# Optimization experiments

Measured on AMD Instinct MI355X. Metric: run time of the kernel, lower is better.

Reference implementation:

```python
import jax, jax.numpy as jnp
import numpy as np

K_PERIODS = 4
PMAX = 64
MIN_PERIOD = 8


def setup_inputs() -> dict:
    key = jax.random.key(0)
    x = jax.random.normal(key, (32, 512, 64), dtype=jnp.float32)  # [B, T, N]
    return {"x": x}


def reference(x):
    """Dense, fixed-shape equivalent of PeriodicityTransform.forward (mask=None).

    Instead of a Python list of variable-shape PeriodGroup tiles, returns a
    padded tensor values[bn, k, c, p] where for each (sequence bn, freq rank k)
    with period P and cycles C, values[bn, k, :C, :P] equals the torch tile
    seqs[bn, T-C*P : T].reshape(C, P); entries outside (C, P) are zero.
    Also returns the integer periods and cycles per (bn, k).
    """
    B, T, N = x.shape
    BN = B * N
    seqs = jnp.transpose(x, (0, 2, 1)).reshape(BN, T)  # [BN, T]

    # top-k nonzero FFT frequencies (DC bin zeroed out)
    spec = jnp.fft.rfft(seqs, axis=-1)
    mag2 = spec.real ** 2 + spec.imag ** 2
    mag2 = mag2.at[..., 0].set(0.0)
    _, kidx = jax.lax.top_k(mag2, K_PERIODS)  # [BN, K]
    kidx = jnp.maximum(kidx, 1)

    # periods = clamp(T // f, min=MIN_PERIOD, max=PMAX); cycles = T // period
    periods = jnp.clip(T // kidx, MIN_PERIOD, PMAX)  # [BN, K]
    cycles = T // periods                              # [BN, K]

    cmax = T // MIN_PERIOD  # static upper bound on cycles
    i = jnp.arange(cmax)[:, None]   # cycle index  [Cmax, 1]
    j = jnp.arange(PMAX)[None, :]   # phase index  [1, Pmax]

    start = T - cycles * periods                                   # [BN, K]
    idx = start[..., None, None] + i * periods[..., None, None] + j  # [BN,K,Cmax,Pmax]
    idx = jnp.clip(idx, 0, T - 1)
    valid = (i < cycles[..., None, None]) & (j < periods[..., None, None])

    gathered = jnp.take_along_axis(
        seqs[:, None, :], idx.reshape(BN, K_PERIODS, -1), axis=-1
    ).reshape(BN, K_PERIODS, cmax, PMAX)
    values = jnp.where(valid, gathered, jnp.float32(0.0))
    return values, periods, cycles
```

## Files before the change

### kernel.cpp

```cpp
#include <hip/hip_runtime.h>
#include <math.h>

#define TT 512
#define KP 4

typedef unsigned long long u64;

#define SYNCL() asm volatile("s_waitcnt lgkmcnt(0)\n\ts_barrier" ::: "memory")
#define SYNCW() do { asm volatile("s_waitcnt lgkmcnt(0)" ::: "memory"); \
                     __builtin_amdgcn_sched_barrier(0); } while (0)

__global__ __launch_bounds__(256) void periodicity_kernel(const float* __restrict__ x,
                                                          float* __restrict__ out) {
    const int bn   = (blockIdx.x & 7) * 256 + (blockIdx.x >> 3);
    const int tid  = threadIdx.x;
    const int lane = tid & 63;
    const int wid  = tid >> 6;
    const int b = bn >> 6;
    const int n = bn & 63;

    __shared__ float2 tw[TT];
    __shared__ __align__(16) float row[TT];
    __shared__ __align__(16) float2 buf[TT];
    __shared__ __align__(16) u64 keys[256];
    __shared__ double candV8[8];

    float sv, cv;
    sincosf((float)(2.0 * M_PI / 512.0) * (float)tid, &sv, &cv);
    tw[tid]       = make_float2(cv, -sv);
    tw[tid + 256] = make_float2(-cv, sv);

    const float* xb = x + (size_t)b * (TT * 64) + n;
    {
        float v0 = xb[(size_t)tid * 64];
        float v1 = xb[(size_t)(tid + 256) * 64];
        row[tid] = v0;  row[tid + 256] = v1;
        float sum = v0 + v1, dif = v0 - v1;
        buf[tid]       = make_float2(sum, 0.f);
        buf[tid + 256] = make_float2(dif * cv, -dif * sv);
    }
    SYNCL();

    if (wid < 2) {
        const int h = wid;
        float2* bb = &buf[h << 8];

        #pragma unroll
        for (int stg = 0; stg < 3; ++stg) {
            const int Q  = 64 >> (2 * stg);
            const int g  = lane >> (6 - 2 * stg);
            const int i  = lane & (Q - 1);
            const int base = g * (Q << 2) + i;
            float2 x0 = bb[base],         x1 = bb[base + Q];
            float2 x2 = bb[base + 2 * Q], x3 = bb[base + 3 * Q];
            float2 A  = make_float2(x0.x + x2.x, x0.y + x2.y);
            float2 Bm = make_float2(x0.x - x2.x, x0.y - x2.y);
            float2 Cc = make_float2(x1.x + x3.x, x1.y + x3.y);
            float2 D  = make_float2(x1.x - x3.x, x1.y - x3.y);
            float2 y0 = make_float2(A.x + Cc.x, A.y + Cc.y);
            float2 y2 = make_float2(A.x - Cc.x, A.y - Cc.y);
            float2 y1 = make_float2(Bm.x + D.y, Bm.y - D.x);
            float2 y3 = make_float2(Bm.x - D.y, Bm.y + D.x);
            const int m = i << (1 + 2 * stg);
            float2 t1 = tw[m], t2 = tw[2 * m], t3 = tw[3 * m];
            bb[base]         = y0;
            bb[base + Q]     = make_float2(y1.x * t1.x - y1.y * t1.y, y1.x * t1.y + y1.y * t1.x);
            bb[base + 2 * Q] = make_float2(y2.x * t2.x - y2.y * t2.y, y2.x * t2.y + y2.y * t2.x);
            bb[base + 3 * Q] = make_float2(y3.x * t3.x - y3.y * t3.y, y3.x * t3.y + y3.y * t3.x);
            SYNCW();
        }

        {
            const int g = lane;
            const int base = g << 2;
            float2 x0 = bb[base],     x1 = bb[base + 1];
            float2 x2 = bb[base + 2], x3 = bb[base + 3];
            float2 A  = make_float2(x0.x + x2.x, x0.y + x2.y);
            float2 Bm = make_float2(x0.x - x2.x, x0.y - x2.y);
            float2 Cc = make_float2(x1.x + x3.x, x1.y + x3.y);
            float2 D  = make_float2(x1.x - x3.x, x1.y - x3.y);
            float2 y0 = make_float2(A.x + Cc.x, A.y + Cc.y);
            float2 y2 = make_float2(A.x - Cc.x, A.y - Cc.y);
            float2 y1 = make_float2(Bm.x + D.y, Bm.y - D.x);
            float2 y3 = make_float2(Bm.x - D.y, Bm.y + D.x);
            const int revg = ((g & 3) << 4) | (((g >> 2) & 3) << 2) | ((g >> 4) & 3);
            const int f0 = 2 * revg + h;
            float m0 = y0.x * y0.x + y0.y * y0.y;
            float m1 = y1.x * y1.x + y1.y * y1.y;
            float m2 = y2.x * y2.x + y2.y * y2.y;
            float m3 = y3.x * y3.x + y3.y * y3.y;
            u64 kA, kB;
            if (f0 == 0) {
                kA = ((u64)__float_as_uint(m1) << 32) | (u64)(256 - 128);
                kB = ((u64)__float_as_uint(m2) << 32) | (u64)(256 - 256);
            } else {
                kA = ((u64)__float_as_uint(m0) << 32) | (u64)(256 - f0);
                kB = ((u64)__float_as_uint(m1) << 32) | (u64)(256 - (f0 + 128));
            }
            ulonglong2* kv = (ulonglong2*)keys;
            kv[(h << 6) + g] = make_ulonglong2(kA, kB);
        }
    }
    SYNCL();

    int   fbin[8];
    float cmag[8];
    {
        const ulonglong2* kv = (const ulonglong2*)keys;
        ulonglong2 p0v = kv[lane * 2];
        ulonglong2 p1v = kv[lane * 2 + 1];
        u64 k0 = p0v.x, k1 = p0v.y, k2 = p1v.x, k3 = p1v.y;
        #define CSWAP(a, b) { if (a < b) { u64 _t = a; a = b; b = _t; } }
        CSWAP(k0, k1) CSWAP(k2, k3) CSWAP(k0, k2) CSWAP(k1, k3) CSWAP(k1, k2)
        #undef CSWAP
        #pragma unroll
        for (int r = 0; r < 8; ++r) {
            u64 w = k0;
            #pragma unroll
            for (int off = 32; off >= 1; off >>= 1) {
                u64 o = __shfl_xor(w, off);
                if (o > w) w = o;
            }
            if (k0 == w) { k0 = k1; k1 = k2; k2 = k3; k3 = 0; }
            fbin[r] = 256 - (int)(w & 0xff);
            cmag[r] = __uint_as_float((unsigned)(w >> 32));
        }
    }

    int per[KP], cycv[KP], stv[KP];
    {
        const bool needRefine =
            ((cmag[0] - cmag[1]) <= 1e-4f * cmag[0]) || ((cmag[1] - cmag[2]) <= 1e-4f * cmag[1]) ||
            ((cmag[2] - cmag[3]) <= 1e-4f * cmag[2]) || ((cmag[3] - cmag[4]) <= 1e-4f * cmag[3]);
        int bins[KP];
        if (!needRefine) {
            #pragma unroll
            for (int k = 0; k < KP; ++k) bins[k] = fbin[k];
        } else {
            {
                const int cid = tid >> 5;
                const int sub = tid & 31;
                int fc;
                switch (cid) {
                    case 0: fc = fbin[0]; break;
                    case 1: fc = fbin[1]; break;
                    case 2: fc = fbin[2]; break;
                    case 3: fc = fbin[3]; break;
                    case 4: fc = fbin[4]; break;
                    case 5: fc = fbin[5]; break;
                    case 6: fc = fbin[6]; break;
                    default: fc = fbin[7]; break;
                }
                const int t0 = sub * 16;
                const double W = 6.2831853071795864769 / 512.0;
                double zr, zi, wr, wi;
                sincos(W * (double)((fc * t0) & 511), &zi, &zr);
                sincos(W * (double)fc, &wi, &wr);
                double ar = 0.0, ai = 0.0;
                const float4* r4 = (const float4*)row;
                #pragma unroll
                for (int v4i = 0; v4i < 4; ++v4i) {
                    float4 xv = r4[sub * 4 + v4i];
                    #define STEP(comp)                                   \
                        { double xd = (double)xv.comp;                   \
                          ar = fma(xd, zr, ar); ai = fma(xd, zi, ai);    \
                          double tq = zr * wr - zi * wi;                 \
                          zi = fma(zr, wi, zi * wr); zr = tq; }
                    STEP(x) STEP(y) STEP(z) STEP(w)
                    #undef STEP
                }
                #pragma unroll
                for (int off = 16; off >= 1; off >>= 1) {
                    ar += __shfl_xor(ar, off);
                    ai += __shfl_xor(ai, off);
                }
                if (sub == 0) candV8[cid] = ar * ar + ai * ai;
            }
            SYNCL();
            unsigned chosen = 0;
            #pragma unroll
            for (int k = 0; k < KP; ++k) {
                double bv = -1.0; int bbin = 0x7fffffff; int bj = 0;
                #pragma unroll
                for (int j = 0; j < 8; ++j) {
                    if (chosen & (1u << j)) continue;
                    double vj = candV8[j];
                    int    bjn = fbin[j];
                    if (vj > bv || (vj == bv && bjn < bbin)) { bv = vj; bbin = bjn; bj = j; }
                }
                chosen |= (1u << bj);
                bins[k] = bbin;
            }
        }
        #pragma unroll
        for (int k = 0; k < KP; ++k) {
            int p = TT / bins[k];
            p = p < 8 ? 8 : (p > 64 ? 64 : p);
            per[k]  = p;
            cycv[k] = TT / p;
            stv[k]  = TT - cycv[k] * p;
        }
    }

    const size_t VOFF = (size_t)2048 * KP * 64 * 64;
    if (tid == 0) {
        #pragma unroll
        for (int k = 0; k < KP; ++k) {
            out[VOFF + (size_t)bn * KP + k]        = (float)per[k];
            out[VOFF + 8192 + (size_t)bn * KP + k] = (float)cycv[k];
        }
    }

    float* outv = out + (size_t)bn * (KP * 64 * 64);
    const int c_local = tid >> 4;
    const int p0 = (tid & 15) << 2;
    #pragma unroll
    for (int it = 0; it < 16; ++it) {
        const int k = it >> 2;
        const int c = ((it & 3) << 4) + c_local;
        float4 v = make_float4(0.f, 0.f, 0.f, 0.f);
        const int P = per[k], C = cycv[k], S0 = stv[k];
        if (c < C) {
            const int base = S0 + c * P;
            if (p0 + 3 < P) {
                v.x = row[base + p0];
                v.y = row[base + p0 + 1];
                v.z = row[base + p0 + 2];
                v.w = row[base + p0 + 3];
            } else {
                if (p0     < P) v.x = row[base + p0];
                if (p0 + 1 < P) v.y = row[base + p0 + 1];
                if (p0 + 2 < P) v.z = row[base + p0 + 2];
                if (p0 + 3 < P) v.w = row[base + p0 + 3];
            }
        }
        *(float4*)(outv + (size_t)it * 1024 + (size_t)tid * 4) = v;
    }
}

extern "C" void kernel_launch(void* const* d_in, const int* in_sizes, int n_in,
                              void* d_out, int out_size, void* d_ws, size_t ws_size,
                              hipStream_t stream) {
    const float* x = (const float*)d_in[0];
    float* out = (float*)d_out;
    hipLaunchKernelGGL(periodicity_kernel, dim3(2048), dim3(256), 0, stream, x, out);
}
```

Baseline: 30.48 us.

## Process four sequences per block with warp-specialized FFT/output software pipeline

Each block now handles four consecutive sequences with 512 threads. Two waves prefetch the next sequence and run the FFT and top-k, while six waves write the output tiles for the previous sequence from double-buffered shared memory. The refinement path is moved into a single wave using shuffles instead of a block barrier. This aims to overlap output stores with FFT compute and amortize twiddle setup, at the cost of fewer blocks (512) and extra barriers per stage.

```diff
diff --git a/kernel.cpp b/kernel.cpp
--- a/kernel.cpp
+++ b/kernel.cpp
@@ -10,136 +10,195 @@
 #define SYNCW() do { asm volatile("s_waitcnt lgkmcnt(0)" ::: "memory"); \
                      __builtin_amdgcn_sched_barrier(0); } while (0)
 
-__global__ __launch_bounds__(256) void periodicity_kernel(const float* __restrict__ x,
-                                                          float* __restrict__ out) {
-    const int bn   = (blockIdx.x & 7) * 256 + (blockIdx.x >> 3);
+__global__ __launch_bounds__(512, 4) void periodicity_kernel(const float* __restrict__ x,
+                                                             float* __restrict__ out) {
+    const int bid  = blockIdx.x;
+    const int blk  = (bid & 7) * 64 + (bid >> 3);
     const int tid  = threadIdx.x;
     const int lane = tid & 63;
     const int wid  = tid >> 6;
-    const int b = bn >> 6;
-    const int n = bn & 63;
 
     __shared__ float2 tw[TT];
-    __shared__ __align__(16) float row[TT];
+    __shared__ __align__(16) float rowl[2][TT];
     __shared__ __align__(16) float2 buf[TT];
     __shared__ __align__(16) u64 keys[256];
-    __shared__ double candV8[8];
-
-    float sv, cv;
-    sincosf((float)(2.0 * M_PI / 512.0) * (float)tid, &sv, &cv);
-    tw[tid]       = make_float2(cv, -sv);
-    tw[tid + 256] = make_float2(-cv, sv);
-
-    const float* xb = x + (size_t)b * (TT * 64) + n;
+    __shared__ int pst[2][12];
+
+    const int b  = blk >> 4;
+    const int n0 = (blk & 15) << 2;
+    const size_t VOFF = (size_t)2048 * KP * 64 * 64;
+
+    float cur[8], nxt[8];
+    const float* xb = x + (size_t)b * (TT * 64);
+    if (wid < 2) {
+        const float* xc = xb + n0;
+        #pragma unroll
+        for (int q = 0; q < 8; ++q) cur[q] = xc[(size_t)(lane + 64 * q) * 64];
+    }
+
     {
-        float v0 = xb[(size_t)tid * 64];
-        float v1 = xb[(size_t)(tid + 256) * 64];
-        row[tid] = v0;  row[tid + 256] = v1;
-        float sum = v0 + v1, dif = v0 - v1;
-        buf[tid]       = make_float2(sum, 0.f);
-        buf[tid + 256] = make_float2(dif * cv, -dif * sv);
+        float s, c;
+        sincosf((float)(2.0 * M_PI / 512.0) * (float)tid, &s, &c);
+        tw[tid] = make_float2(c, -s);
     }
     SYNCL();
 
-    if (wid < 2) {
-        const int h = wid;
-        float2* bb = &buf[h << 8];
-
-        #pragma unroll
-        for (int stg = 0; stg < 3; ++stg) {
-            const int Q  = 64 >> (2 * stg);
-            const int g  = lane >> (6 - 2 * stg);
-            const int i  = lane & (Q - 1);
-            const int base = g * (Q << 2) + i;
-            float2 x0 = bb[base],         x1 = bb[base + Q];
-            float2 x2 = bb[base + 2 * Q], x3 = bb[base + 3 * Q];
-            float2 A  = make_float2(x0.x + x2.x, x0.y + x2.y);
-            float2 Bm = make_float2(x0.x - x2.x, x0.y - x2.y);
-            float2 Cc = make_float2(x1.x + x3.x, x1.y + x3.y);
-            float2 D  = make_float2(x1.x - x3.x, x1.y - x3.y);
-            float2 y0 = make_float2(A.x + Cc.x, A.y + Cc.y);
-            float2 y2 = make_float2(A.x - Cc.x, A.y - Cc.y);
-            float2 y1 = make_float2(Bm.x + D.y, Bm.y - D.x);
-            float2 y3 = make_float2(Bm.x - D.y, Bm.y + D.x);
-            const int m = i << (1 + 2 * stg);
-            float2 t1 = tw[m], t2 = tw[2 * m], t3 = tw[3 * m];
-            bb[base]         = y0;
-            bb[base + Q]     = make_float2(y1.x * t1.x - y1.y * t1.y, y1.x * t1.y + y1.y * t1.x);
-            bb[base + 2 * Q] = make_float2(y2.x * t2.x - y2.y * t2.y, y2.x * t2.y + y2.y * t2.x);
-            bb[base + 3 * Q] = make_float2(y3.x * t3.x - y3.y * t3.y, y3.x * t3.y + y3.y * t3.x);
+    for (int r = 0; r < 5; ++r) {
+        const int slot = r & 1, pslot = slot ^ 1;
+
+        if (wid < 2 && r < 4) {
+            const int h = wid;
+            if (r < 3) {
+                const float* xc = xb + (n0 + r + 1);
+                #pragma unroll
+                for (int q = 0; q < 8; ++q) nxt[q] = xc[(size_t)(lane + 64 * q) * 64];
+            }
+            if (h == 0) {
+                #pragma unroll
+                for (int q = 0; q < 4; ++q) rowl[slot][lane + 64 * q] = cur[q];
+            } else {
+                #pragma unroll
+                for (int q = 0; q < 4; ++q) rowl[slot][256 + lane + 64 * q] = cur[4 + q];
+            }
+            if (h == 0) {
+                #pragma unroll
+                for (int q = 0; q < 4; ++q)
+                    buf[lane + 64 * q] = make_float2(cur[q] + cur[4 + q], 0.f);
+            } else {
+                #pragma unroll
+                for (int q = 0; q < 4; ++q) {
+                    const int j = lane + 64 * q;
+                    float dif = cur[q] - cur[4 + q];
+                    float2 t = tw[j];
+                    buf[256 + j] = make_float2(dif * t.x, dif * t.y);
+                }
+            }
             SYNCW();
-        }
-
-        {
-            const int g = lane;
-            const int base = g << 2;
-            float2 x0 = bb[base],     x1 = bb[base + 1];
-            float2 x2 = bb[base + 2], x3 = bb[base + 3];
-            float2 A  = make_float2(x0.x + x2.x, x0.y + x2.y);
-            float2 Bm = make_float2(x0.x - x2.x, x0.y - x2.y);
-            float2 Cc = make_float2(x1.x + x3.x, x1.y + x3.y);
-            float2 D  = make_float2(x1.x - x3.x, x1.y - x3.y);
-            float2 y0 = make_float2(A.x + Cc.x, A.y + Cc.y);
-            float2 y2 = make_float2(A.x - Cc.x, A.y - Cc.y);
-            float2 y1 = make_float2(Bm.x + D.y, Bm.y - D.x);
-            float2 y3 = make_float2(Bm.x - D.y, Bm.y + D.x);
-            const int revg = ((g & 3) << 4) | (((g >> 2) & 3) << 2) | ((g >> 4) & 3);
-            const int f0 = 2 * revg + h;
-            float m0 = y0.x * y0.x + y0.y * y0.y;
-            float m1 = y1.x * y1.x + y1.y * y1.y;
-            float m2 = y2.x * y2.x + y2.y * y2.y;
-            float m3 = y3.x * y3.x + y3.y * y3.y;
-            u64 kA, kB;
-            if (f0 == 0) {
-                kA = ((u64)__float_as_uint(m1) << 32) | (u64)(256 - 128);
-                kB = ((u64)__float_as_uint(m2) << 32) | (u64)(256 - 256);
+
+            float2* bb = &buf[h << 8];
+            #pragma unroll
+            for (int stg = 0; stg < 3; ++stg) {
+                const int Q  = 64 >> (2 * stg);
+                const int g  = lane >> (6 - 2 * stg);
+                const int i  = lane & (Q - 1);
+                const int base = g * (Q << 2) + i;
+                float2 x0 = bb[base],         x1 = bb[base + Q];
+                float2 x2 = bb[base + 2 * Q], x3 = bb[base + 3 * Q];
+                float2 A  = make_float2(x0.x + x2.x, x0.y + x2.y);
+                float2 Bm = make_float2(x0.x - x2.x, x0.y - x2.y);
+                float2 Cc = make_float2(x1.x + x3.x, x1.y + x3.y);
+                float2 D  = make_float2(x1.x - x3.x, x1.y - x3.y);
+                float2 y0 = make_float2(A.x + Cc.x, A.y + Cc.y);
+                float2 y2 = make_float2(A.x - Cc.x, A.y - Cc.y);
+                float2 y1 = make_float2(Bm.x + D.y, Bm.y - D.x);
+                float2 y3 = make_float2(Bm.x - D.y, Bm.y + D.x);
+                const int m = i << (1 + 2 * stg);
+                float2 t1 = tw[m], t2 = tw[2 * m], t3 = tw[3 * m];
+                bb[base]         = y0;
+                bb[base + Q]     = make_float2(y1.x * t1.x - y1.y * t1.y, y1.x * t1.y + y1.y * t1.x);
+                bb[base + 2 * Q] = make_float2(y2.x * t2.x - y2.y * t2.y, y2.x * t2.y + y2.y * t2.x);
+                bb[base + 3 * Q] = make_float2(y3.x * t3.x - y3.y * t3.y, y3.x * t3.y + y3.y * t3.x);
+                SYNCW();
+            }
+
+            {
+                const int g = lane;
+                const int base = g << 2;
+                float2 x0 = bb[base],     x1 = bb[base + 1];
+                float2 x2 = bb[base + 2], x3 = bb[base + 3];
+                float2 A  = make_float2(x0.x + x2.x, x0.y + x2.y);
+                float2 Bm = make_float2(x0.x - x2.x, x0.y - x2.y);
+                float2 Cc = make_float2(x1.x + x3.x, x1.y + x3.y);
+                float2 D  = make_float2(x1.x - x3.x, x1.y - x3.y);
+                float2 y0 = make_float2(A.x + Cc.x, A.y + Cc.y);
+                float2 y2 = make_float2(A.x - Cc.x, A.y - Cc.y);
+                float2 y1 = make_float2(Bm.x + D.y, Bm.y - D.x);
+                float2 y3 = make_float2(Bm.x - D.y, Bm.y + D.x);
+                const int revg = ((g & 3) << 4) | (((g >> 2) & 3) << 2) | ((g >> 4) & 3);
+                const int f0 = 2 * revg + h;
+                float m0 = y0.x * y0.x + y0.y * y0.y;
+                float m1 = y1.x * y1.x + y1.y * y1.y;
+                float m2 = y2.x * y2.x + y2.y * y2.y;
+                u64 kA, kB;
+                if (f0 == 0) {
+                    kA = ((u64)__float_as_uint(m1) << 32) | (u64)(256 - 128);
+                    kB = ((u64)__float_as_uint(m2) << 32) | (u64)(256 - 256);
+                } else {
+                    kA = ((u64)__float_as_uint(m0) << 32) | (u64)(256 - f0);
+                    kB = ((u64)__float_as_uint(m1) << 32) | (u64)(256 - (f0 + 128));
+                }
+                ((ulonglong2*)keys)[(h << 6) + g] = make_ulonglong2(kA, kB);
+            }
+        }
+
+        if (wid >= 2 && r >= 1) {
+            const int bnp = b * 64 + n0 + (r - 1);
+            float* outv = out + (size_t)bnp * (KP * 64 * 64);
+            const int idx0 = (wid - 2) * 64 + lane;
+            #pragma unroll
+            for (int k2 = 0; k2 < 2; ++k2) {
+                const int P = pst[pslot][k2], C = pst[pslot][4 + k2], S0 = pst[pslot][8 + k2];
+                for (int i = idx0; i < 1024; i += 384) {
+                    const int c  = i >> 4;
+                    const int p0 = (i & 15) << 2;
+                    float4 v = make_float4(0.f, 0.f, 0.f, 0.f);
+                    if (c < C) {
+                        const int base = S0 + c * P;
+                        if (p0 + 3 < P) {
+                            v.x = rowl[pslot][base + p0];
+                            v.y = rowl[pslot][base + p0 + 1];
+                            v.z = rowl[pslot][base + p0 + 2];
+                            v.w = rowl[pslot][base + p0 + 3];
+                        } else {
+                            if (p0     < P) v.x = rowl[pslot][base + p0];
+                            if (p0 + 1 < P) v.y = rowl[pslot][base + p0 + 1];
+                            if (p0 + 2 < P) v.z = rowl[pslot][base + p0 + 2];
+                            if (p0 + 3 < P) v.w = rowl[pslot][base + p0 + 3];
+                        }
+                    }
+                    *(float4*)(outv + (size_t)k2 * 4096 + (size_t)i * 4) = v;
+                }
+            }
+        }
+
+        SYNCL();
+
+        if (wid == 0 && r < 4) {
+            int   fbin[8];
+            float cmag[8];
+            {
+                const ulonglong2* kv = (const ulonglong2*)keys;
+                ulonglong2 p0v = kv[lane * 2];
+                ulonglong2 p1v = kv[lane * 2 + 1];
+                u64 k0 = p0v.x, k1 = p0v.y, k2 = p1v.x, k3 = p1v.y;
+                #define CSWAP(a, b) { if (a < b) { u64 _t = a; a = b; b = _t; } }
+                CSWAP(k0, k1) CSWAP(k2, k3) CSWAP(k0, k2) CSWAP(k1, k3) CSWAP(k1, k2)
+                #undef CSWAP
+                #pragma unroll
+                for (int rr = 0; rr < 8; ++rr) {
+                    u64 w = k0;
+                    #pragma unroll
+                    for (int off = 32; off >= 1; off >>= 1) {
+                        u64 o = __shfl_xor(w, off);
+                        if (o > w) w = o;
+                    }
+                    if (k0 == w) { k0 = k1; k1 = k2; k2 = k3; k3 = 0; }
+                    fbin[rr] = 256 - (int)(w & 0xff);
+                    cmag[rr] = __uint_as_float((unsigned)(w >> 32));
+                }
+            }
+
+            const bool needRefine =
+                ((cmag[0] - cmag[1]) <= 1e-4f * cmag[0]) || ((cmag[1] - cmag[2]) <= 1e-4f * cmag[1]) ||
+                ((cmag[2] - cmag[3]) <= 1e-4f * cmag[2]) || ((cmag[3] - cmag[4]) <= 1e-4f * cmag[3]);
+
+            int bins[KP];
+            if (!needRefine) {
+                #pragma unroll
+                for (int k = 0; k < KP; ++k) bins[k] = fbin[k];
             } else {
-                kA = ((u64)__float_as_uint(m0) << 32) | (u64)(256 - f0);
-                kB = ((u64)__float_as_uint(m1) << 32) | (u64)(256 - (f0 + 128));
-            }
-            ulonglong2* kv = (ulonglong2*)keys;
-            kv[(h << 6) + g] = make_ulonglong2(kA, kB);
-        }
-    }
-    SYNCL();
-
-    int   fbin[8];
-    float cmag[8];
-    {
-        const ulonglong2* kv = (const ulonglong2*)keys;
-        ulonglong2 p0v = kv[lane * 2];
-        ulonglong2 p1v = kv[lane * 2 + 1];
-        u64 k0 = p0v.x, k1 = p0v.y, k2 = p1v.x, k3 = p1v.y;
-        #define CSWAP(a, b) { if (a < b) { u64 _t = a; a = b; b = _t; } }
-        CSWAP(k0, k1) CSWAP(k2, k3) CSWAP(k0, k2) CSWAP(k1, k3) CSWAP(k1, k2)
-        #undef CSWAP
-        #pragma unroll
-        for (int r = 0; r < 8; ++r) {
-            u64 w = k0;
-            #pragma unroll
-            for (int off = 32; off >= 1; off >>= 1) {
-                u64 o = __shfl_xor(w, off);
-                if (o > w) w = o;
-            }
-            if (k0 == w) { k0 = k1; k1 = k2; k2 = k3; k3 = 0; }
-            fbin[r] = 256 - (int)(w & 0xff);
-            cmag[r] = __uint_as_float((unsigned)(w >> 32));
-        }
-    }
-
-    int per[KP], cycv[KP], stv[KP];
-    {
-        const bool needRefine =
-            ((cmag[0] - cmag[1]) <= 1e-4f * cmag[0]) || ((cmag[1] - cmag[2]) <= 1e-4f * cmag[1]) ||
-            ((cmag[2] - cmag[3]) <= 1e-4f * cmag[2]) || ((cmag[3] - cmag[4]) <= 1e-4f * cmag[3]);
-        int bins[KP];
-        if (!needRefine) {
-            #pragma unroll
-            for (int k = 0; k < KP; ++k) bins[k] = fbin[k];
-        } else {
-            {
-                const int cid = tid >> 5;
-                const int sub = tid & 31;
+                const int cid = lane >> 3;
+                const int sub = lane & 7;
                 int fc;
                 switch (cid) {
                     case 0: fc = fbin[0]; break;
@@ -151,16 +210,16 @@
                     case 6: fc = fbin[6]; break;
                     default: fc = fbin[7]; break;
                 }
-                const int t0 = sub * 16;
+                const int t0 = sub * 64;
                 const double W = 6.2831853071795864769 / 512.0;
                 double zr, zi, wr, wi;
                 sincos(W * (double)((fc * t0) & 511), &zi, &zr);
                 sincos(W * (double)fc, &wi, &wr);
                 double ar = 0.0, ai = 0.0;
-                const float4* r4 = (const float4*)row;
-                #pragma unroll
-                for (int v4i = 0; v4i < 4; ++v4i) {
-                    float4 xv = r4[sub * 4 + v4i];
+                const float4* r4 = (const float4*)rowl[slot];
+                #pragma unroll
+                for (int v4i = 0; v4i < 16; ++v4i) {
+                    float4 xv = r4[sub * 16 + v4i];
                     #define STEP(comp)                                   \
                         { double xd = (double)xv.comp;                   \
                           ar = fma(xd, zr, ar); ai = fma(xd, zi, ai);    \
@@ -170,71 +229,80 @@
                     #undef STEP
                 }
                 #pragma unroll
-                for (int off = 16; off >= 1; off >>= 1) {
+                for (int off = 4; off >= 1; off >>= 1) {
                     ar += __shfl_xor(ar, off);
                     ai += __shfl_xor(ai, off);
                 }
-                if (sub == 0) candV8[cid] = ar * ar + ai * ai;
-            }
-            SYNCL();
-            unsigned chosen = 0;
+                double Vg = ar * ar + ai * ai;
+                double V[8];
+                #pragma unroll
+                for (int j = 0; j < 8; ++j) V[j] = __shfl(Vg, j * 8);
+                unsigned chosen = 0;
+                #pragma unroll
+                for (int k = 0; k < KP; ++k) {
+                    double bv = -1.0; int bbin = 0x7fffffff; int bj = 0;
+                    #pragma unroll
+                    for (int j = 0; j < 8; ++j) {
+                        if (chosen & (1u << j)) continue;
+                        if (V[j] > bv || (V[j] == bv && fbin[j] < bbin)) { bv = V[j]; bbin = fbin[j]; bj = j; }
+                    }
+                    chosen |= (1u << bj);
+                    bins[k] = bbin;
+                }
+            }
+
+            const int bn = b * 64 + n0 + r;
+            if (lane == 0) {
+                #pragma unroll
+                for (int k = 0; k < KP; ++k) {
+                    int p = TT / bins[k];
+                    p = p < 8 ? 8 : (p > 64 ? 64 : p);
+                    const int cy = TT / p;
+                    pst[slot][k]     = p;
+                    pst[slot][4 + k] = cy;
+                    pst[slot][8 + k] = TT - cy * p;
+                    out[VOFF + (size_t)bn * KP + k]        = (float)p;
+                    out[VOFF + 8192 + (size_t)bn * KP + k] = (float)cy;
+                }
+            }
+        }
+
+        if (wid >= 2 && r >= 1) {
+            const int bnp = b * 64 + n0 + (r - 1);
+            float* outv = out + (size_t)bnp * (KP * 64 * 64);
+            const int idx0 = (wid - 2) * 64 + lane;
             #pragma unroll
-            for (int k = 0; k < KP; ++k) {
-                double bv = -1.0; int bbin = 0x7fffffff; int bj = 0;
-                #pragma unroll
-                for (int j = 0; j < 8; ++j) {
-                    if (chosen & (1u << j)) continue;
-                    double vj = candV8[j];
-                    int    bjn = fbin[j];
-                    if (vj > bv || (vj == bv && bjn < bbin)) { bv = vj; bbin = bjn; bj = j; }
-                }
-                chosen |= (1u << bj);
-                bins[k] = bbin;
-            }
-        }
-        #pragma unroll
-        for (int k = 0; k < KP; ++k) {
-            int p = TT / bins[k];
-            p = p < 8 ? 8 : (p > 64 ? 64 : p);
-            per[k]  = p;
-            cycv[k] = TT / p;
-            stv[k]  = TT - cycv[k] * p;
-        }
-    }
-
-    const size_t VOFF = (size_t)2048 * KP * 64 * 64;
-    if (tid == 0) {
-        #pragma unroll
-        for (int k = 0; k < KP; ++k) {
-            out[VOFF + (size_t)bn * KP + k]        = (float)per[k];
-            out[VOFF + 8192 + (size_t)bn * KP + k] = (float)cycv[k];
-        }
-    }
-
-    float* outv = out + (size_t)bn * (KP * 64 * 64);
-    const int c_local = tid >> 4;
-    const int p0 = (tid & 15) << 2;
-    #pragma unroll
-    for (int it = 0; it < 16; ++it) {
-        const int k = it >> 2;
-        const int c = ((it & 3) << 4) + c_local;
-        float4 v = make_float4(0.f, 0.f, 0.f, 0.f);
-        const int P = per[k], C = cycv[k], S0 = stv[k];
-        if (c < C) {
-            const int base = S0 + c * P;
-            if (p0 + 3 < P) {
-                v.x = row[base + p0];
-                v.y = row[base + p0 + 1];
-                v.z = row[base + p0 + 2];
-                v.w = row[base + p0 + 3];
-            } else {
-                if (p0     < P) v.x = row[base + p0];
-                if (p0 + 1 < P) v.y = row[base + p0 + 1];
-                if (p0 + 2 < P) v.z = row[base + p0 + 2];
-                if (p0 + 3 < P) v.w = row[base + p0 + 3];
-            }
-        }
-        *(float4*)(outv + (size_t)it * 1024 + (size_t)tid * 4) = v;
+            for (int k2 = 2; k2 < 4; ++k2) {
+                const int P = pst[pslot][k2], C = pst[pslot][4 + k2], S0 = pst[pslot][8 + k2];
+                for (int i = idx0; i < 1024; i += 384) {
+                    const int c  = i >> 4;
+                    const int p0 = (i & 15) << 2;
+                    float4 v = make_float4(0.f, 0.f, 0.f, 0.f);
+                    if (c < C) {
+                        const int base = S0 + c * P;
+                        if (p0 + 3 < P) {
+                            v.x = rowl[pslot][base + p0];
+                            v.y = rowl[pslot][base + p0 + 1];
+                            v.z = rowl[pslot][base + p0 + 2];
+                            v.w = rowl[pslot][base + p0 + 3];
+                        } else {
+                            if (p0     < P) v.x = rowl[pslot][base + p0];
+                            if (p0 + 1 < P) v.y = rowl[pslot][base + p0 + 1];
+                            if (p0 + 2 < P) v.z = rowl[pslot][base + p0 + 2];
+                            if (p0 + 3 < P) v.w = rowl[pslot][base + p0 + 3];
+                        }
+                    }
+                    *(float4*)(outv + (size_t)k2 * 4096 + (size_t)i * 4) = v;
+                }
+            }
+        }
+
+        SYNCL();
+
+        if (wid < 2 && r < 4) {
+            #pragma unroll
+            for (int q = 0; q < 8; ++q) cur[q] = nxt[q];
+        }
     }
 }
 
@@ -243,5 +311,5 @@
                               hipStream_t stream) {
     const float* x = (const float*)d_in[0];
     float* out = (float*)d_out;
-    hipLaunchKernelGGL(periodicity_kernel, dim3(2048), dim3(256), 0, stream, x, out);
+    hipLaunchKernelGGL(periodicity_kernel, dim3(512), dim3(512), 0, stream, x, out);
 }
```

Result: slower. 35.39 us (+16.1%).

## Add pre-transpose kernel so periodicity kernel reads contiguous rows

Applied to the files above, without the earlier changes.

Adds a separate transpose kernel that writes x into a [BN, T] workspace layout. The main kernel then reads each sequence contiguously instead of doing stride-64 gathers. This replaces uncoalesced loads with coalesced ones, at the cost of a second kernel launch and an extra 4 MB write and read through the workspace. If the workspace is too small, the kernel falls back to the original strided path.

```diff
diff --git a/kernel.cpp b/kernel.cpp
--- a/kernel.cpp
+++ b/kernel.cpp
@@ -10,9 +10,42 @@
 #define SYNCW() do { asm volatile("s_waitcnt lgkmcnt(0)" ::: "memory"); \
                      __builtin_amdgcn_sched_barrier(0); } while (0)
 
+__global__ __launch_bounds__(256) void transpose_kernel(const float* __restrict__ x,
+                                                        float* __restrict__ xt) {
+    __shared__ float tile[64][65];
+    const int b  = blockIdx.x >> 3;
+    const int t0 = (blockIdx.x & 7) << 6;
+    const int j  = threadIdx.x;
+    #pragma unroll
+    for (int it = 0; it < 4; ++it) {
+        const int flat = it * 256 + j;
+        const int trow = flat >> 4, f4c = flat & 15;
+        float4 v = *(const float4*)(x + (size_t)(b * 512 + t0 + trow) * 64 + f4c * 4);
+        tile[trow][f4c * 4 + 0] = v.x;
+        tile[trow][f4c * 4 + 1] = v.y;
+        tile[trow][f4c * 4 + 2] = v.z;
+        tile[trow][f4c * 4 + 3] = v.w;
+    }
+    __syncthreads();
+    #pragma unroll
+    for (int it = 0; it < 4; ++it) {
+        const int flat = it * 256 + j;
+        const int nrow = flat >> 4, f4c = flat & 15;
+        float4 v;
+        v.x = tile[f4c * 4 + 0][nrow];
+        v.y = tile[f4c * 4 + 1][nrow];
+        v.z = tile[f4c * 4 + 2][nrow];
+        v.w = tile[f4c * 4 + 3][nrow];
+        *(float4*)(xt + (size_t)(b * 64 + nrow) * 512 + t0 + f4c * 4) = v;
+    }
+}
+
 __global__ __launch_bounds__(256) void periodicity_kernel(const float* __restrict__ x,
-                                                          float* __restrict__ out) {
-    const int bn   = (blockIdx.x & 7) * 256 + (blockIdx.x >> 3);
+                                                          const float* __restrict__ xt,
+                                                          float* __restrict__ out,
+                                                          int transposed) {
+    const int bn   = transposed ? (int)blockIdx.x
+                                : ((blockIdx.x & 7) * 256 + (blockIdx.x >> 3));
     const int tid  = threadIdx.x;
     const int lane = tid & 63;
     const int wid  = tid >> 6;
@@ -30,10 +63,17 @@
     tw[tid]       = make_float2(cv, -sv);
     tw[tid + 256] = make_float2(-cv, sv);
 
-    const float* xb = x + (size_t)b * (TT * 64) + n;
     {
-        float v0 = xb[(size_t)tid * 64];
-        float v1 = xb[(size_t)(tid + 256) * 64];
+        float v0, v1;
+        if (transposed) {
+            const float* xr = xt + (size_t)bn * TT;
+            v0 = xr[tid];
+            v1 = xr[tid + 256];
+        } else {
+            const float* xb = x + (size_t)b * (TT * 64) + n;
+            v0 = xb[(size_t)tid * 64];
+            v1 = xb[(size_t)(tid + 256) * 64];
+        }
         row[tid] = v0;  row[tid + 256] = v1;
         float sum = v0 + v1, dif = v0 - v1;
         buf[tid]       = make_float2(sum, 0.f);
@@ -88,7 +128,6 @@
             float m0 = y0.x * y0.x + y0.y * y0.y;
             float m1 = y1.x * y1.x + y1.y * y1.y;
             float m2 = y2.x * y2.x + y2.y * y2.y;
-            float m3 = y3.x * y3.x + y3.y * y3.y;
             u64 kA, kB;
             if (f0 == 0) {
                 kA = ((u64)__float_as_uint(m1) << 32) | (u64)(256 - 128);
@@ -97,8 +136,7 @@
                 kA = ((u64)__float_as_uint(m0) << 32) | (u64)(256 - f0);
                 kB = ((u64)__float_as_uint(m1) << 32) | (u64)(256 - (f0 + 128));
             }
-            ulonglong2* kv = (ulonglong2*)keys;
-            kv[(h << 6) + g] = make_ulonglong2(kA, kB);
+            ((ulonglong2*)keys)[(h << 6) + g] = make_ulonglong2(kA, kB);
         }
     }
     SYNCL();
@@ -243,5 +281,12 @@
                               hipStream_t stream) {
     const float* x = (const float*)d_in[0];
     float* out = (float*)d_out;
-    hipLaunchKernelGGL(periodicity_kernel, dim3(2048), dim3(256), 0, stream, x, out);
+    const size_t xt_bytes = (size_t)2048 * 512 * sizeof(float);
+    if (ws_size >= xt_bytes) {
+        float* xt = (float*)d_ws;
+        hipLaunchKernelGGL(transpose_kernel, dim3(256), dim3(256), 0, stream, x, xt);
+        hipLaunchKernelGGL(periodicity_kernel, dim3(2048), dim3(256), 0, stream, x, xt, out, 1);
+    } else {
+        hipLaunchKernelGGL(periodicity_kernel, dim3(2048), dim3(256), 0, stream, x, (const float*)nullptr, out, 0);
+    }
 }
```

Result: slower. 35.87 us (+17.7%).

## Process two adjacent sequences per block to coalesce input loads

Applied to the files above, without the earlier changes.

Each block now handles two consecutive (b,n) sequences, loading both columns up front so the strided input reads cover adjacent addresses. The grid is halved and the FFT/top-k/scatter pipeline runs twice per block in a loop, with the twiddles computed once and reused. The aim is better use of each fetched input line and less per-block setup. In exchange each block does serial work for two sequences and the grid has fewer blocks, which may reduce latency hiding. The old blockIdx swizzle is also dropped.

```diff
diff --git a/kernel.cpp b/kernel.cpp
--- a/kernel.cpp
+++ b/kernel.cpp
@@ -12,12 +12,10 @@
 
 __global__ __launch_bounds__(256) void periodicity_kernel(const float* __restrict__ x,
                                                           float* __restrict__ out) {
-    const int bn   = (blockIdx.x & 7) * 256 + (blockIdx.x >> 3);
+    const int blk  = blockIdx.x;
     const int tid  = threadIdx.x;
     const int lane = tid & 63;
     const int wid  = tid >> 6;
-    const int b = bn >> 6;
-    const int n = bn & 63;
 
     __shared__ float2 tw[TT];
     __shared__ __align__(16) float row[TT];
@@ -30,211 +28,225 @@
     tw[tid]       = make_float2(cv, -sv);
     tw[tid + 256] = make_float2(-cv, sv);
 
-    const float* xb = x + (size_t)b * (TT * 64) + n;
-    {
-        float v0 = xb[(size_t)tid * 64];
-        float v1 = xb[(size_t)(tid + 256) * 64];
-        row[tid] = v0;  row[tid + 256] = v1;
-        float sum = v0 + v1, dif = v0 - v1;
-        buf[tid]       = make_float2(sum, 0.f);
-        buf[tid + 256] = make_float2(dif * cv, -dif * sv);
-    }
-    SYNCL();
-
-    if (wid < 2) {
-        const int h = wid;
-        float2* bb = &buf[h << 8];
-
+    const int bn0 = blk * 2;
+    const float* xb0 = x + (size_t)(bn0 >> 6) * (TT * 64) + (bn0 & 63);
+    const float* xb1 = xb0 + 1;
+    float a0 = xb0[(size_t)tid * 64];
+    float a1 = xb0[(size_t)(tid + 256) * 64];
+    float b0 = xb1[(size_t)tid * 64];
+    float b1 = xb1[(size_t)(tid + 256) * 64];
+
+    const size_t VOFF = (size_t)2048 * KP * 64 * 64;
+
+    #pragma unroll
+    for (int r = 0; r < 2; ++r) {
+        const int bn = bn0 + r;
+        const float v0 = r ? b0 : a0;
+        const float v1 = r ? b1 : a1;
+
+        SYNCL();
+
+        {
+            row[tid] = v0;  row[tid + 256] = v1;
+            float sum = v0 + v1, dif = v0 - v1;
+            float2 t = tw[tid];
+            buf[tid]       = make_float2(sum, 0.f);
+            buf[tid + 256] = make_float2(dif * t.x, dif * t.y);
+        }
+        SYNCL();
+
+        if (wid < 2) {
+            const int h = wid;
+            float2* bb = &buf[h << 8];
+
+            #pragma unroll
+            for (int stg = 0; stg < 3; ++stg) {
+                const int Q  = 64 >> (2 * stg);
+                const int g  = lane >> (6 - 2 * stg);
+                const int i  = lane & (Q - 1);
+                const int base = g * (Q << 2) + i;
+                float2 x0 = bb[base],         x1 = bb[base + Q];
+                float2 x2 = bb[base + 2 * Q], x3 = bb[base + 3 * Q];
+                float2 A  = make_float2(x0.x + x2.x, x0.y + x2.y);
+                float2 Bm = make_float2(x0.x - x2.x, x0.y - x2.y);
+                float2 Cc = make_float2(x1.x + x3.x, x1.y + x3.y);
+                float2 D  = make_float2(x1.x - x3.x, x1.y - x3.y);
+                float2 y0 = make_float2(A.x + Cc.x, A.y + Cc.y);
+                float2 y2 = make_float2(A.x - Cc.x, A.y - Cc.y);
+                float2 y1 = make_float2(Bm.x + D.y, Bm.y - D.x);
+                float2 y3 = make_float2(Bm.x - D.y, Bm.y + D.x);
+                const int m = i << (1 + 2 * stg);
+                float2 t1 = tw[m], t2 = tw[2 * m], t3 = tw[3 * m];
+                bb[base]         = y0;
+                bb[base + Q]     = make_float2(y1.x * t1.x - y1.y * t1.y, y1.x * t1.y + y1.y * t1.x);
+                bb[base + 2 * Q] = make_float2(y2.x * t2.x - y2.y * t2.y, y2.x * t2.y + y2.y * t2.x);
+                bb[base + 3 * Q] = make_float2(y3.x * t3.x - y3.y * t3.y, y3.x * t3.y + y3.y * t3.x);
+                SYNCW();
+            }
+
+            {
+                const int g = lane;
+                const int base = g << 2;
+                float2 x0 = bb[base],     x1 = bb[base + 1];
+                float2 x2 = bb[base + 2], x3 = bb[base + 3];
+                float2 A  = make_float2(x0.x + x2.x, x0.y + x2.y);
+                float2 Bm = make_float2(x0.x - x2.x, x0.y - x2.y);
+                float2 Cc = make_float2(x1.x + x3.x, x1.y + x3.y);
+                float2 D  = make_float2(x1.x - x3.x, x1.y - x3.y);
+                float2 y0 = make_float2(A.x + Cc.x, A.y + Cc.y);
+                float2 y2 = make_float2(A.x - Cc.x, A.y - Cc.y);
+                float2 y1 = make_float2(Bm.x + D.y, Bm.y - D.x);
+                float2 y3 = make_float2(Bm.x - D.y, Bm.y + D.x);
+                const int revg = ((g & 3) << 4) | (((g >> 2) & 3) << 2) | ((g >> 4) & 3);
+                const int f0 = 2 * revg + h;
+                float m0 = y0.x * y0.x + y0.y * y0.y;
+                float m1 = y1.x * y1.x + y1.y * y1.y;
+                float m2 = y2.x * y2.x + y2.y * y2.y;
+                u64 kA, kB;
+                if (f0 == 0) {
+                    kA = ((u64)__float_as_uint(m1) << 32) | (u64)(256 - 128);
+                    kB = ((u64)__float_as_uint(m2) << 32) | (u64)(256 - 256);
+                } else {
+                    kA = ((u64)__float_as_uint(m0) << 32) | (u64)(256 - f0);
+                    kB = ((u64)__float_as_uint(m1) << 32) | (u64)(256 - (f0 + 128));
+                }
+                ((ulonglong2*)keys)[(h << 6) + g] = make_ulonglong2(kA, kB);
+            }
+        }
+        SYNCL();
+
+        int   fbin[8];
+        float cmag[8];
+        {
+            const ulonglong2* kv = (const ulonglong2*)keys;
+            ulonglong2 p0v = kv[lane * 2];
+            ulonglong2 p1v = kv[lane * 2 + 1];
+            u64 k0 = p0v.x, k1 = p0v.y, k2 = p1v.x, k3 = p1v.y;
+            #define CSWAP(a, b) { if (a < b) { u64 _t = a; a = b; b = _t; } }
+            CSWAP(k0, k1) CSWAP(k2, k3) CSWAP(k0, k2) CSWAP(k1, k3) CSWAP(k1, k2)
+            #undef CSWAP
+            #pragma unroll
+            for (int rr = 0; rr < 8; ++rr) {
+                u64 w = k0;
+                #pragma unroll
+                for (int off = 32; off >= 1; off >>= 1) {
+                    u64 o = __shfl_xor(w, off);
+                    if (o > w) w = o;
+                }
+                if (k0 == w) { k0 = k1; k1 = k2; k2 = k3; k3 = 0; }
+                fbin[rr] = 256 - (int)(w & 0xff);
+                cmag[rr] = __uint_as_float((unsigned)(w >> 32));
+            }
+        }
+
+        int per[KP], cycv[KP], stv[KP];
+        {
+            const bool needRefine =
+                ((cmag[0] - cmag[1]) <= 1e-4f * cmag[0]) || ((cmag[1] - cmag[2]) <= 1e-4f * cmag[1]) ||
+                ((cmag[2] - cmag[3]) <= 1e-4f * cmag[2]) || ((cmag[3] - cmag[4]) <= 1e-4f * cmag[3]);
+            int bins[KP];
+            if (!needRefine) {
+                #pragma unroll
+                for (int k = 0; k < KP; ++k) bins[k] = fbin[k];
+            } else {
+                {
+                    const int cid = tid >> 5;
+                    const int sub = tid & 31;
+                    int fc;
+                    switch (cid) {
+                        case 0: fc = fbin[0]; break;
+                        case 1: fc = fbin[1]; break;
+                        case 2: fc = fbin[2]; break;
+                        case 3: fc = fbin[3]; break;
+                        case 4: fc = fbin[4]; break;
+                        case 5: fc = fbin[5]; break;
+                        case 6: fc = fbin[6]; break;
+                        default: fc = fbin[7]; break;
+                    }
+                    const int t0 = sub * 16;
+                    const double W = 6.2831853071795864769 / 512.0;
+                    double zr, zi, wr, wi;
+                    sincos(W * (double)((fc * t0) & 511), &zi, &zr);
+                    sincos(W * (double)fc, &wi, &wr);
+                    double ar = 0.0, ai = 0.0;
+                    const float4* r4 = (const float4*)row;
+                    #pragma unroll
+                    for (int v4i = 0; v4i < 4; ++v4i) {
+                        float4 xv = r4[sub * 4 + v4i];
+                        #define STEP(comp)                                   \
+                            { double xd = (double)xv.comp;                   \
+                              ar = fma(xd, zr, ar); ai = fma(xd, zi, ai);    \
+                              double tq = zr * wr - zi * wi;                 \
+                              zi = fma(zr, wi, zi * wr); zr = tq; }
+                        STEP(x) STEP(y) STEP(z) STEP(w)
+                        #undef STEP
+                    }
+                    #pragma unroll
+                    for (int off = 16; off >= 1; off >>= 1) {
+                        ar += __shfl_xor(ar, off);
+                        ai += __shfl_xor(ai, off);
+                    }
+                    if (sub == 0) candV8[cid] = ar * ar + ai * ai;
+                }
+                SYNCL();
+                unsigned chosen = 0;
+                #pragma unroll
+                for (int k = 0; k < KP; ++k) {
+                    double bv = -1.0; int bbin = 0x7fffffff; int bj = 0;
+                    #pragma unroll
+                    for (int j = 0; j < 8; ++j) {
+                        if (chosen & (1u << j)) continue;
+                        double vj = candV8[j];
+                        int    bjn = fbin[j];
+                        if (vj > bv || (vj == bv && bjn < bbin)) { bv = vj; bbin = bjn; bj = j; }
+                    }
+                    chosen |= (1u << bj);
+                    bins[k] = bbin;
+                }
+            }
+            #pragma unroll
+            for (int k = 0; k < KP; ++k) {
+                int p = TT / bins[k];
+                p = p < 8 ? 8 : (p > 64 ? 64 : p);
+                per[k]  = p;
+                cycv[k] = TT / p;
+                stv[k]  = TT - cycv[k] * p;
+            }
+        }
+
+        if (tid == 0) {
+            #pragma unroll
+            for (int k = 0; k < KP; ++k) {
+                out[VOFF + (size_t)bn * KP + k]        = (float)per[k];
+                out[VOFF + 8192 + (size_t)bn * KP + k] = (float)cycv[k];
+            }
+        }
+
+        float* outv = out + (size_t)bn * (KP * 64 * 64);
+        const int c_local = tid >> 4;
+        const int p0 = (tid & 15) << 2;
         #pragma unroll
-        for (int stg = 0; stg < 3; ++stg) {
-            const int Q  = 64 >> (2 * stg);
-            const int g  = lane >> (6 - 2 * stg);
-            const int i  = lane & (Q - 1);
-            const int base = g * (Q << 2) + i;
-            float2 x0 = bb[base],         x1 = bb[base + Q];
-            float2 x2 = bb[base + 2 * Q], x3 = bb[base + 3 * Q];
-            float2 A  = make_float2(x0.x + x2.x, x0.y + x2.y);
-            float2 Bm = make_float2(x0.x - x2.x, x0.y - x2.y);
-            float2 Cc = make_float2(x1.x + x3.x, x1.y + x3.y);
-            float2 D  = make_float2(x1.x - x3.x, x1.y - x3.y);
-            float2 y0 = make_float2(A.x + Cc.x, A.y + Cc.y);
-            float2 y2 = make_float2(A.x - Cc.x, A.y - Cc.y);
-            float2 y1 = make_float2(Bm.x + D.y, Bm.y - D.x);
-            float2 y3 = make_float2(Bm.x - D.y, Bm.y + D.x);
-            const int m = i << (1 + 2 * stg);
-            float2 t1 = tw[m], t2 = tw[2 * m], t3 = tw[3 * m];
-            bb[base]         = y0;
-            bb[base + Q]     = make_float2(y1.x * t1.x - y1.y * t1.y, y1.x * t1.y + y1.y * t1.x);
-            bb[base + 2 * Q] = make_float2(y2.x * t2.x - y2.y * t2.y, y2.x * t2.y + y2.y * t2.x);
-            bb[base + 3 * Q] = make_float2(y3.x * t3.x - y3.y * t3.y, y3.x * t3.y + y3.y * t3.x);
-            SYNCW();
-        }
-
-        {
-            const int g = lane;
-            const int base = g << 2;
-            float2 x0 = bb[base],     x1 = bb[base + 1];
-            float2 x2 = bb[base + 2], x3 = bb[base + 3];
-            float2 A  = make_float2(x0.x + x2.x, x0.y + x2.y);
-            float2 Bm = make_float2(x0.x - x2.x, x0.y - x2.y);
-            float2 Cc = make_float2(x1.x + x3.x, x1.y + x3.y);
-            float2 D  = make_float2(x1.x - x3.x, x1.y - x3.y);
-            float2 y0 = make_float2(A.x + Cc.x, A.y + Cc.y);
-            float2 y2 = make_float2(A.x - Cc.x, A.y - Cc.y);
-            float2 y1 = make_float2(Bm.x + D.y, Bm.y - D.x);
-            float2 y3 = make_float2(Bm.x - D.y, Bm.y + D.x);
-            const int revg = ((g & 3) << 4) | (((g >> 2) & 3) << 2) | ((g >> 4) & 3);
-            const int f0 = 2 * revg + h;
-            float m0 = y0.x * y0.x + y0.y * y0.y;
-            float m1 = y1.x * y1.x + y1.y * y1.y;
-            float m2 = y2.x * y2.x + y2.y * y2.y;
-            float m3 = y3.x * y3.x + y3.y * y3.y;
-            u64 kA, kB;
-            if (f0 == 0) {
-                kA = ((u64)__float_as_uint(m1) << 32) | (u64)(256 - 128);
-                kB = ((u64)__float_as_uint(m2) << 32) | (u64)(256 - 256);
-            } else {
-                kA = ((u64)__float_as_uint(m0) << 32) | (u64)(256 - f0);
-                kB = ((u64)__float_as_uint(m1) << 32) | (u64)(256 - (f0 + 128));
-            }
-            ulonglong2* kv = (ulonglong2*)keys;
-            kv[(h << 6) + g] = make_ulonglong2(kA, kB);
-        }
-    }
-    SYNCL();
-
-    int   fbin[8];
-    float cmag[8];
-    {
-        const ulonglong2* kv = (const ulonglong2*)keys;
-        ulonglong2 p0v = kv[lane * 2];
-        ulonglong2 p1v = kv[lane * 2 + 1];
-        u64 k0 = p0v.x, k1 = p0v.y, k2 = p1v.x, k3 = p1v.y;
-        #define CSWAP(a, b) { if (a < b) { u64 _t = a; a = b; b = _t; } }
-        CSWAP(k0, k1) CSWAP(k2, k3) CSWAP(k0, k2) CSWAP(k1, k3) CSWAP(k1, k2)
-        #undef CSWAP
-        #pragma unroll
-        for (int r = 0; r < 8; ++r) {
-            u64 w = k0;
-            #pragma unroll
-            for (int off = 32; off >= 1; off >>= 1) {
-                u64 o = __shfl_xor(w, off);
-                if (o > w) w = o;
-            }
-            if (k0 == w) { k0 = k1; k1 = k2; k2 = k3; k3 = 0; }
-            fbin[r] = 256 - (int)(w & 0xff);
-            cmag[r] = __uint_as_float((unsigned)(w >> 32));
-        }
-    }
-
-    int per[KP], cycv[KP], stv[KP];
-    {
-        const bool needRefine =
-            ((cmag[0] - cmag[1]) <= 1e-4f * cmag[0]) || ((cmag[1] - cmag[2]) <= 1e-4f * cmag[1]) ||
-            ((cmag[2] - cmag[3]) <= 1e-4f * cmag[2]) || ((cmag[3] - cmag[4]) <= 1e-4f * cmag[3]);
-        int bins[KP];
-        if (!needRefine) {
-            #pragma unroll
-            for (int k = 0; k < KP; ++k) bins[k] = fbin[k];
-        } else {
-            {
-                const int cid = tid >> 5;
-                const int sub = tid & 31;
-                int fc;
-                switch (cid) {
-                    case 0: fc = fbin[0]; break;
-                    case 1: fc = fbin[1]; break;
-                    case 2: fc = fbin[2]; break;
-                    case 3: fc = fbin[3]; break;
-                    case 4: fc = fbin[4]; break;
-                    case 5: fc = fbin[5]; break;
-                    case 6: fc = fbin[6]; break;
-                    default: fc = fbin[7]; break;
-                }
-                const int t0 = sub * 16;
-                const double W = 6.2831853071795864769 / 512.0;
-                double zr, zi, wr, wi;
-                sincos(W * (double)((fc * t0) & 511), &zi, &zr);
-                sincos(W * (double)fc, &wi, &wr);
-                double ar = 0.0, ai = 0.0;
-                const float4* r4 = (const float4*)row;
-                #pragma unroll
-                for (int v4i = 0; v4i < 4; ++v4i) {
-                    float4 xv = r4[sub * 4 + v4i];
-                    #define STEP(comp)                                   \
-                        { double xd = (double)xv.comp;                   \
-                          ar = fma(xd, zr, ar); ai = fma(xd, zi, ai);    \
-                          double tq = zr * wr - zi * wi;                 \
-                          zi = fma(zr, wi, zi * wr); zr = tq; }
-                    STEP(x) STEP(y) STEP(z) STEP(w)
-                    #undef STEP
-                }
-                #pragma unroll
-                for (int off = 16; off >= 1; off >>= 1) {
-                    ar += __shfl_xor(ar, off);
-                    ai += __shfl_xor(ai, off);
-                }
-                if (sub == 0) candV8[cid] = ar * ar + ai * ai;
-            }
-            SYNCL();
-            unsigned chosen = 0;
-            #pragma unroll
-            for (int k = 0; k < KP; ++k) {
-                double bv = -1.0; int bbin = 0x7fffffff; int bj = 0;
-                #pragma unroll
-                for (int j = 0; j < 8; ++j) {
-                    if (chosen & (1u << j)) continue;
-                    double vj = candV8[j];
-                    int    bjn = fbin[j];
-                    if (vj > bv || (vj == bv && bjn < bbin)) { bv = vj; bbin = bjn; bj = j; }
-                }
-                chosen |= (1u << bj);
-                bins[k] = bbin;
-            }
-        }
-        #pragma unroll
-        for (int k = 0; k < KP; ++k) {
-            int p = TT / bins[k];
-            p = p < 8 ? 8 : (p > 64 ? 64 : p);
-            per[k]  = p;
-            cycv[k] = TT / p;
-            stv[k]  = TT - cycv[k] * p;
-        }
-    }
-
-    const size_t VOFF = (size_t)2048 * KP * 64 * 64;
-    if (tid == 0) {
-        #pragma unroll
-        for (int k = 0; k < KP; ++k) {
-            out[VOFF + (size_t)bn * KP + k]        = (float)per[k];
-            out[VOFF + 8192 + (size_t)bn * KP + k] = (float)cycv[k];
-        }
-    }
-
-    float* outv = out + (size_t)bn * (KP * 64 * 64);
-    const int c_local = tid >> 4;
-    const int p0 = (tid & 15) << 2;
-    #pragma unroll
-    for (int it = 0; it < 16; ++it) {
-        const int k = it >> 2;
-        const int c = ((it & 3) << 4) + c_local;
-        float4 v = make_float4(0.f, 0.f, 0.f, 0.f);
-        const int P = per[k], C = cycv[k], S0 = stv[k];
-        if (c < C) {
-            const int base = S0 + c * P;
-            if (p0 + 3 < P) {
-                v.x = row[base + p0];
-                v.y = row[base + p0 + 1];
-                v.z = row[base + p0 + 2];
-                v.w = row[base + p0 + 3];
-            } else {
-                if (p0     < P) v.x = row[base + p0];
-                if (p0 + 1 < P) v.y = row[base + p0 + 1];
-                if (p0 + 2 < P) v.z = row[base + p0 + 2];
-                if (p0 + 3 < P) v.w = row[base + p0 + 3];
-            }
-        }
-        *(float4*)(outv + (size_t)it * 1024 + (size_t)tid * 4) = v;
+        for (int it = 0; it < 16; ++it) {
+            const int k = it >> 2;
+            const int c = ((it & 3) << 4) + c_local;
+            float4 v = make_float4(0.f, 0.f, 0.f, 0.f);
+            const int P = per[k], C = cycv[k], S0 = stv[k];
+            if (c < C) {
+                const int base = S0 + c * P;
+                if (p0 + 3 < P) {
+                    v.x = row[base + p0];
+                    v.y = row[base + p0 + 1];
+                    v.z = row[base + p0 + 2];
+                    v.w = row[base + p0 + 3];
+                } else {
+                    if (p0     < P) v.x = row[base + p0];
+                    if (p0 + 1 < P) v.y = row[base + p0 + 1];
+                    if (p0 + 2 < P) v.z = row[base + p0 + 2];
+                    if (p0 + 3 < P) v.w = row[base + p0 + 3];
+                }
+            }
+            *(float4*)(outv + (size_t)it * 1024 + (size_t)tid * 4) = v;
+        }
     }
 }
 
@@ -243,5 +255,5 @@
                               hipStream_t stream) {
     const float* x = (const float*)d_in[0];
     float* out = (float*)d_out;
-    hipLaunchKernelGGL(periodicity_kernel, dim3(2048), dim3(256), 0, stream, x, out);
+    hipLaunchKernelGGL(periodicity_kernel, dim3(1024), dim3(256), 0, stream, x, out);
 }
```

After: 33.42 us. 1.1x slower.
